# Performance work log

Measured on AMD Instinct MI355X. Metric: run time of the kernel, lower is better.

Reference implementation:

```python
import jax, jax.numpy as jnp
import numpy as np

N_VISIBLE = 50000
N_HIDDEN = 5000
N_NODES = N_VISIBLE + N_HIDDEN
N_EDGES = 1_000_000
BATCH = 128


def setup_inputs() -> dict:
    key = jax.random.key(0)
    k1, k2, k3, k4, k5 = jax.random.split(key, 5)
    # parameters, initialized as in the torch module
    linear = 0.05 * (2.0 * jax.random.uniform(k1, (N_NODES,), dtype=jnp.float32) - 1.0)
    quadratic = 5.0 * (2.0 * jax.random.uniform(k2, (N_EDGES,), dtype=jnp.float32) - 1.0)
    # bipartite visible-hidden edges -> CSR-like flat buffers (via segment ids)
    flat_adj = jax.random.randint(k3, (N_EDGES,), 0, N_VISIBLE, dtype=jnp.int32).astype(jnp.int64)  # visible endpoint per edge
    seg_ids = jax.random.randint(k4, (N_EDGES,), 0, N_HIDDEN, dtype=jnp.int32).astype(jnp.int64)    # hidden bin per edge
    flat_j_idx = jnp.arange(N_EDGES, dtype=jnp.int64)  # quadratic coefficient index per flat entry
    hidden_idx = jnp.arange(N_HIDDEN, dtype=jnp.int64) + N_VISIBLE
    # observed spin configurations in {0,1} (mapped to +-1 inside reference)
    s = jax.random.randint(k5, (BATCH, N_NODES), 0, 2, dtype=jnp.int32)
    return {
        "linear": linear,
        "quadratic": quadratic,
        "s": s,
        "flat_adj": flat_adj,
        "flat_j_idx": flat_j_idx,
        "seg_ids": seg_ids,
        "hidden_idx": hidden_idx,
        "n_hidden": N_HIDDEN,
    }


def reference(linear, quadratic, s, flat_adj, flat_j_idx, seg_ids, hidden_idx, n_hidden):
    """Per-hidden-unit effective field + conditional spin expectation.

    eff[b, k] = linear[hidden_idx[k]]
                + sum_{e : seg_ids[e]==k} quadratic[flat_j_idx[e]] * s_pm[b, flat_adj[e]]
    returns tanh(-eff)  (conditional expectation of hidden spins given visibles)
    """
    s_pm = (2 * s - 1).astype(linear.dtype)                 # {0,1} -> {-1,+1}, (B, N)
    w = quadratic[flat_j_idx]                               # (E,)
    contrib = s_pm[:, flat_adj].T * w[:, None]              # (E, B) gathered neighbor terms
    field = jax.ops.segment_sum(contrib, seg_ids, num_segments=n_hidden)  # (K, B)
    eff = field.T + linear[hidden_idx][None, :]             # (B, K)
    return jnp.tanh(-eff)
```

## Files before the change

kernel.cpp:

```cpp
#include <hip/hip_runtime.h>
#include <math.h>
#include <stdint.h>

#define NV 50000
#define NH 5000
#define NN 55000
#define NB 128
#define NG 8
#define SUBSLOT 64
#define MAXREC 512


__global__ void __launch_bounds__(256) pack_scatter_kernel(
        const int* __restrict__ s, uint32_t* __restrict__ bits,
        const int4* __restrict__ adj4, const int4* __restrict__ seg4,
        const float4* __restrict__ quad4,
        uint32_t* __restrict__ cursors, uint2* __restrict__ recs,
        int packBlocks, int E4) {
    int blk = blockIdx.x;
    if (blk < packBlocks) {
        int tid = blk * 256 + threadIdx.x;
        int v = tid >> 2;
        int g = tid & 3;
        if (v >= NV) return;
        const int* col = s + (size_t)g * 32 * NN + v;
        uint32_t w = 0;
#pragma unroll
        for (int j = 0; j < 32; ++j)
            w |= (uint32_t)(col[(size_t)j * NN] & 1) << j;
        bits[(size_t)v * 4 + g] = w;
    } else {
        int t = (blk - packBlocks) * 256 + threadIdx.x;
        if (t >= E4) return;
        const int g = blk & (NG - 1);
        uint32_t* gcur = cursors + (size_t)g * NH;
        uint2* grecs = recs + (size_t)g * NH * SUBSLOT;
        int4 a  = adj4[t];
        int4 sg = seg4[t];
        float4 w = quad4[t];
        uint32_t p0 = atomicAdd(&gcur[sg.x], 1u);
        uint32_t p1 = atomicAdd(&gcur[sg.y], 1u);
        uint32_t p2 = atomicAdd(&gcur[sg.z], 1u);
        uint32_t p3 = atomicAdd(&gcur[sg.w], 1u);
        if (p0 < SUBSLOT) grecs[(size_t)sg.x * SUBSLOT + p0] = make_uint2((uint32_t)a.x, __float_as_uint(w.x));
        if (p1 < SUBSLOT) grecs[(size_t)sg.y * SUBSLOT + p1] = make_uint2((uint32_t)a.y, __float_as_uint(w.y));
        if (p2 < SUBSLOT) grecs[(size_t)sg.z * SUBSLOT + p2] = make_uint2((uint32_t)a.z, __float_as_uint(w.z));
        if (p3 < SUBSLOT) grecs[(size_t)sg.w * SUBSLOT + p3] = make_uint2((uint32_t)a.w, __float_as_uint(w.w));
    }
}

__global__ void __launch_bounds__(256) field_tanh_kernel(
        const uint32_t* __restrict__ cursors,
        const uint2* __restrict__ recs,
        const uint4* __restrict__ bits4,
        const float* __restrict__ linear,
        float* __restrict__ out) {
    int g8 = blockIdx.x & 7;
    int m = blockIdx.x >> 3;
    int pair = m + 313 * g8;
    if (pair >= NH / 2) return;
    int k0 = pair * 2;
    int tid = threadIdx.x;

    __shared__ __align__(16) uint32_t rows[2][5][MAXREC];
    __shared__ float part[2][256];

    int T8s[2];
#pragma unroll
    for (int kk = 0; kk < 2; ++kk) {
        int k = k0 + kk;
        int c[NG], offs[NG], T = 0;
#pragma unroll
        for (int g = 0; g < NG; ++g) {
            int cg = (int)cursors[(size_t)g * NH + k];
            if (cg > SUBSLOT) cg = SUBSLOT;
            c[g] = cg;
            offs[g] = T;
            T += cg;
        }
        int T8 = (T + 7) & ~7;
        T8s[kk] = T8;
        for (int i = T + tid; i < T8; i += 256) rows[kk][4][i] = 0u;
        for (int t = tid; t < T; t += 256) {
            int rem = t, g = 0;
            while (rem >= c[g]) { rem -= c[g]; ++g; }
            uint2 r = recs[((size_t)g * NH + k) * SUBSLOT + rem];
            uint4 mw = bits4[r.x];
            rows[kk][0][t] = mw.x;
            rows[kk][1][t] = mw.y;
            rows[kk][2][t] = mw.z;
            rows[kk][3][t] = mw.w;
            rows[kk][4][t] = r.y;
        }
    }
    __syncthreads();

    int b = tid & 127;
    int grp = tid >> 7;
    const int bsh = b & 31;
    const int widx = b >> 5;
#pragma unroll
    for (int kk = 0; kk < 2; ++kk) {
        const uint32_t* mrow = rows[kk][widx];
        const uint32_t* wrow = rows[kk][4];
        float a0 = 0.f, a1 = 0.f, a2 = 0.f, a3 = 0.f;
        for (int i = grp * 4; i < T8s[kk]; i += 8) {
            uint4 mm = *(const uint4*)(mrow + i);
            uint4 ww = *(const uint4*)(wrow + i);
            float f0 = __uint_as_float(ww.x);
            float f1 = __uint_as_float(ww.y);
            float f2 = __uint_as_float(ww.z);
            float f3 = __uint_as_float(ww.w);
            a0 += ((mm.x >> bsh) & 1u) ? f0 : -f0;
            a1 += ((mm.y >> bsh) & 1u) ? f1 : -f1;
            a2 += ((mm.z >> bsh) & 1u) ? f2 : -f2;
            a3 += ((mm.w >> bsh) & 1u) ? f3 : -f3;
        }
        part[kk][tid] = (a0 + a1) + (a2 + a3);
    }
    __syncthreads();
    if (tid < 128) {
        float e0 = part[0][tid] + part[0][tid + 128] + linear[NV + k0];
        float e1 = part[1][tid] + part[1][tid + 128] + linear[NV + k0 + 1];
        float2 o = make_float2(tanhf(-e0), tanhf(-e1));
        *(float2*)(out + (size_t)tid * NH + k0) = o;
    }
}

extern "C" void kernel_launch(void* const* d_in, const int* in_sizes, int n_in,
                              void* d_out, int out_size, void* d_ws, size_t ws_size,
                              hipStream_t stream) {
    const float* linear = (const float*)d_in[0];
    const float* quad   = (const float*)d_in[1];
    const int*   s      = (const int*)d_in[2];
    const int*   adj    = (const int*)d_in[3];
    const int*   seg    = (const int*)d_in[5];
    const int E = in_sizes[5];
    float* out = (float*)d_out;

    char* ws = (char*)d_ws;
    uint32_t* bits    = (uint32_t*)(ws);
    uint32_t* cursors = (uint32_t*)(ws + 800000);
    uint2*    recs    = (uint2*)   (ws + 960000);

    hipMemsetAsync(cursors, 0, NH * NG * sizeof(uint32_t), stream);
    const int E4 = E / 4;
    const int packBlocks = (NV * 4 + 255) / 256;
    const int scatBlocks = (E4 + 255) / 256;
    pack_scatter_kernel<<<packBlocks + scatBlocks, 256, 0, stream>>>(
        s, bits, (const int4*)adj, (const int4*)seg, (const float4*)quad,
        cursors, recs, packBlocks, E4);
    field_tanh_kernel<<<313 * 8, 256, 0, stream>>>(cursors, recs, (const uint4*)bits,
                                                   linear, out);
}
```

Baseline: 155.3 us.

## Partition edge scatter by XCD-owned hidden ranges with per-hidden single slots

Replaces the 8-way sub-slotted scatter with a persistent scatter kernel in which each block reads its XCD id and claims edge chunks through a per-range chunk counter. Each range owns 625 hidden units, so the atomics on a given counter mostly come from one XCD's L2, and records land in one contiguous slot per hidden unit. The memset is folded into the pack kernel, and the field kernel drops the multi-group offset walk. In exchange, every range pass rereads all segment ids (eight full passes over seg), and pack and scatter now run as separate launches instead of overlapping in one.

```diff
diff --git a/kernel.cpp b/kernel.cpp
--- a/kernel.cpp
+++ b/kernel.cpp
@@ -6,51 +6,71 @@
 #define NH 5000
 #define NN 55000
 #define NB 128
-#define NG 8
-#define SUBSLOT 64
-#define MAXREC 512
+#define SLOT 320
+#define KRANGE 625
+#define CS 4096
 
 
-__global__ void __launch_bounds__(256) pack_scatter_kernel(
+__global__ void __launch_bounds__(256) pack_zero_kernel(
         const int* __restrict__ s, uint32_t* __restrict__ bits,
-        const int4* __restrict__ adj4, const int4* __restrict__ seg4,
-        const float4* __restrict__ quad4,
-        uint32_t* __restrict__ cursors, uint2* __restrict__ recs,
-        int packBlocks, int E4) {
-    int blk = blockIdx.x;
-    if (blk < packBlocks) {
-        int tid = blk * 256 + threadIdx.x;
-        int v = tid >> 2;
-        int g = tid & 3;
-        if (v >= NV) return;
-        const int* col = s + (size_t)g * 32 * NN + v;
-        uint32_t w = 0;
+        uint32_t* __restrict__ zero_region) {
+    if (blockIdx.x == 0) {
+        for (int i = threadIdx.x; i < NH + 8; i += 256) zero_region[i] = 0u;
+    }
+    int tid = blockIdx.x * 256 + threadIdx.x;
+    int v = tid >> 2;
+    int g = tid & 3;
+    if (v >= NV) return;
+    const int* col = s + (size_t)g * 32 * NN + v;
+    uint32_t w = 0;
 #pragma unroll
-        for (int j = 0; j < 32; ++j)
-            w |= (uint32_t)(col[(size_t)j * NN] & 1) << j;
-        bits[(size_t)v * 4 + g] = w;
-    } else {
-        int t = (blk - packBlocks) * 256 + threadIdx.x;
-        if (t >= E4) return;
-        const int g = blk & (NG - 1);
-        uint32_t* gcur = cursors + (size_t)g * NH;
-        uint2* grecs = recs + (size_t)g * NH * SUBSLOT;
-        int4 a  = adj4[t];
-        int4 sg = seg4[t];
-        float4 w = quad4[t];
-        uint32_t p0 = atomicAdd(&gcur[sg.x], 1u);
-        uint32_t p1 = atomicAdd(&gcur[sg.y], 1u);
-        uint32_t p2 = atomicAdd(&gcur[sg.z], 1u);
-        uint32_t p3 = atomicAdd(&gcur[sg.w], 1u);
-        if (p0 < SUBSLOT) grecs[(size_t)sg.x * SUBSLOT + p0] = make_uint2((uint32_t)a.x, __float_as_uint(w.x));
-        if (p1 < SUBSLOT) grecs[(size_t)sg.y * SUBSLOT + p1] = make_uint2((uint32_t)a.y, __float_as_uint(w.y));
-        if (p2 < SUBSLOT) grecs[(size_t)sg.z * SUBSLOT + p2] = make_uint2((uint32_t)a.z, __float_as_uint(w.z));
-        if (p3 < SUBSLOT) grecs[(size_t)sg.w * SUBSLOT + p3] = make_uint2((uint32_t)a.w, __float_as_uint(w.w));
+    for (int j = 0; j < 32; ++j)
+        w |= (uint32_t)(col[(size_t)j * NN] & 1) << j;
+    bits[(size_t)v * 4 + g] = w;
+}
+
+__global__ void __launch_bounds__(256) scatter_xcd_kernel(
+        const int4* __restrict__ seg4, const int* __restrict__ adj,
+        const float* __restrict__ quad,
+        uint32_t* __restrict__ cnt_k, uint32_t* __restrict__ chunk_cnt,
+        uint2* __restrict__ recs, int E4, int nchunk) {
+    uint32_t xcc = (uint32_t)__builtin_amdgcn_s_getreg((3 << 11) | 20) & 7u;
+    __shared__ int sh_c;
+    for (int gi = 0; gi < 8; ++gi) {
+        int gg = (int)((xcc + gi) & 7u);
+        const int klo = gg * KRANGE, khi = klo + KRANGE;
+        while (true) {
+            if (threadIdx.x == 0) sh_c = (int)atomicAdd(&chunk_cnt[gg], 1u);
+            __syncthreads();
+            int c = sh_c;
+            __syncthreads();
+            if (c >= nchunk) break;
+            int base4 = c * (CS / 4);
+#pragma unroll
+            for (int j = 0; j < CS / 1024; ++j) {
+                int t4 = base4 + j * 256 + (int)threadIdx.x;
+                if (t4 >= E4) continue;
+                int4 sg = seg4[t4];
+                int e0 = t4 * 4;
+#pragma unroll
+                for (int cmp = 0; cmp < 4; ++cmp) {
+                    int k = (cmp == 0) ? sg.x : (cmp == 1) ? sg.y : (cmp == 2) ? sg.z : sg.w;
+                    if (k >= klo && k < khi) {
+                        int e = e0 + cmp;
+                        uint32_t v = (uint32_t)adj[e];
+                        float w = quad[e];
+                        uint32_t pos = atomicAdd(&cnt_k[k], 1u);
+                        if (pos < SLOT)
+                            recs[(size_t)k * SLOT + pos] = make_uint2(v, __float_as_uint(w));
+                    }
+                }
+            }
+        }
     }
 }
 
 __global__ void __launch_bounds__(256) field_tanh_kernel(
-        const uint32_t* __restrict__ cursors,
+        const uint32_t* __restrict__ cnt_k,
         const uint2* __restrict__ recs,
         const uint4* __restrict__ bits4,
         const float* __restrict__ linear,
@@ -62,29 +82,20 @@
     int k0 = pair * 2;
     int tid = threadIdx.x;
 
-    __shared__ __align__(16) uint32_t rows[2][5][MAXREC];
+    __shared__ __align__(16) uint32_t rows[2][5][SLOT];
     __shared__ float part[2][256];
 
     int T8s[2];
 #pragma unroll
     for (int kk = 0; kk < 2; ++kk) {
         int k = k0 + kk;
-        int c[NG], offs[NG], T = 0;
-#pragma unroll
-        for (int g = 0; g < NG; ++g) {
-            int cg = (int)cursors[(size_t)g * NH + k];
-            if (cg > SUBSLOT) cg = SUBSLOT;
-            c[g] = cg;
-            offs[g] = T;
-            T += cg;
-        }
+        int T = (int)cnt_k[k];
+        if (T > SLOT) T = SLOT;
         int T8 = (T + 7) & ~7;
         T8s[kk] = T8;
         for (int i = T + tid; i < T8; i += 256) rows[kk][4][i] = 0u;
         for (int t = tid; t < T; t += 256) {
-            int rem = t, g = 0;
-            while (rem >= c[g]) { rem -= c[g]; ++g; }
-            uint2 r = recs[((size_t)g * NH + k) * SUBSLOT + rem];
+            uint2 r = recs[(size_t)k * SLOT + t];
             uint4 mw = bits4[r.x];
             rows[kk][0][t] = mw.x;
             rows[kk][1][t] = mw.y;
@@ -139,17 +150,16 @@
     float* out = (float*)d_out;
 
     char* ws = (char*)d_ws;
-    uint32_t* bits    = (uint32_t*)(ws);
-    uint32_t* cursors = (uint32_t*)(ws + 800000);
-    uint2*    recs    = (uint2*)   (ws + 960000);
+    uint32_t* bits      = (uint32_t*)(ws);
+    uint32_t* cnt_k     = (uint32_t*)(ws + 800000);
+    uint32_t* chunk_cnt = (uint32_t*)(ws + 820000);
+    uint2*    recs      = (uint2*)   (ws + 820032);
 
-    hipMemsetAsync(cursors, 0, NH * NG * sizeof(uint32_t), stream);
     const int E4 = E / 4;
-    const int packBlocks = (NV * 4 + 255) / 256;
-    const int scatBlocks = (E4 + 255) / 256;
-    pack_scatter_kernel<<<packBlocks + scatBlocks, 256, 0, stream>>>(
-        s, bits, (const int4*)adj, (const int4*)seg, (const float4*)quad,
-        cursors, recs, packBlocks, E4);
-    field_tanh_kernel<<<313 * 8, 256, 0, stream>>>(cursors, recs, (const uint4*)bits,
+    const int nchunk = (E + CS - 1) / CS;
+    pack_zero_kernel<<<(NV * 4 + 255) / 256, 256, 0, stream>>>(s, bits, cnt_k);
+    scatter_xcd_kernel<<<1024, 256, 0, stream>>>((const int4*)seg, adj, quad,
+                                                 cnt_k, chunk_cnt, recs, E4, nchunk);
+    field_tanh_kernel<<<313 * 8, 256, 0, stream>>>(cnt_k, recs, (const uint4*)bits,
                                                    linear, out);
 }
```

Result: slower. 279.8 us (+80.2%).
